# Performance work log

Measured on AMD Instinct MI355X. Metric: run time of the kernel, lower is better.

## Reference

```python
import jax, jax.numpy as jnp
import numpy as np


def setup_inputs() -> dict:
    key = jax.random.key(0)
    k1, k2 = jax.random.split(key)
    N, D, T = 1_000_000, 128, 1_000_000
    triplets = jax.random.randint(k1, (T, 3), 0, N, dtype=jnp.int64)
    node_emb = jax.random.normal(k2, (N, D), dtype=jnp.float32)
    vars = jnp.zeros((1,), dtype=jnp.float32)  # unused by forward (parity with original signature)
    return {"triplets": triplets, "node_emb": node_emb, "vars": vars}


def reference(triplets, node_emb, vars) -> jnp.ndarray:
    # gather left/right node embeddings, per-triplet dot product -> [T]
    left = node_emb[triplets[:, 0]]   # [T, D]
    right = node_emb[triplets[:, 2]]  # [T, D]
    scores = jnp.einsum('td,td->t', left, right)
    return scores
```

## Files before the change

### kernel.cpp

```cpp
#include <hip/hip_runtime.h>
#include <hip/hip_bf16.h>

constexpr int U = 8;

__global__ __launch_bounds__(256) void dot_gather_kernel(
    const int* __restrict__ trip,
    const float* __restrict__ emb,
    float* __restrict__ out,
    int T) {
  int gid = blockIdx.x * blockDim.x + threadIdx.x;
  int group = gid >> 5;
  int lane = gid & 31;
  long long t0 = (long long)group * U;
  if (t0 >= T) return;

  int iL[U], iR[U];
  #pragma unroll
  for (int u = 0; u < U; ++u) {
    long long t = (t0 + u < T) ? (t0 + u) : (long long)(T - 1);
    iL[u] = trip[3 * t];
    iR[u] = trip[3 * t + 2];
  }

  float4 a[U], b[U];
  #pragma unroll
  for (int u = 0; u < U; ++u) {
    a[u] = ((const float4*)(emb + (long long)iL[u] * 128))[lane];
    b[u] = ((const float4*)(emb + (long long)iR[u] * 128))[lane];
  }

  #pragma unroll
  for (int u = 0; u < U; ++u) {
    float s = a[u].x * b[u].x + a[u].y * b[u].y + a[u].z * b[u].z + a[u].w * b[u].w;
    #pragma unroll
    for (int off = 16; off > 0; off >>= 1)
      s += __shfl_down(s, off, 32);
    if (lane == 0 && t0 + u < T) out[t0 + u] = s;
  }
}

extern "C" void kernel_launch(void* const* d_in, const int* in_sizes, int n_in,
                              void* d_out, int out_size, void* d_ws, size_t ws_size,
                              hipStream_t stream) {
  const int* trip = (const int*)d_in[0];
  const float* emb = (const float*)d_in[1];
  float* out = (float*)d_out;

  int T = in_sizes[0] / 3;
  long long groups = ((long long)T + U - 1) / U;
  long long total_threads = groups * 32;
  int block = 256;
  long long grid = (total_threads + block - 1) / block;

  dot_gather_kernel<<<(int)grid, block, 0, stream>>>(trip, emb, out, T);
}
```

Baseline: 700.4 us.

## Convert embedding table to fp16 in workspace, then gather half-width rows

Adds a pre-pass that streams the full fp32 embedding table into an fp16 copy in workspace. The dot-product kernel then gathers 256-byte half rows, using 16 lanes per triplet instead of 32, and accumulates in fp32. The aim is to halve the random-gather traffic, which is the main cost. In exchange, every call pays a full-table read plus write in the conversion pass and loses input precision to fp16. There is an fp32 fallback path when workspace is too small.

```diff
diff --git a/kernel.cpp b/kernel.cpp
--- a/kernel.cpp
+++ b/kernel.cpp
@@ -1,17 +1,36 @@
 #include <hip/hip_runtime.h>
-#include <hip/hip_bf16.h>
+
+typedef _Float16 half8 __attribute__((ext_vector_type(8)));
+typedef float floatx4 __attribute__((ext_vector_type(4)));
 
 constexpr int U = 8;
 
-__global__ __launch_bounds__(256) void dot_gather_kernel(
+__global__ __launch_bounds__(256) void convert_f32_f16(
+    const float* __restrict__ emb, _Float16* __restrict__ h, long long n8) {
+  long long i = (long long)blockIdx.x * blockDim.x + threadIdx.x;
+  long long stride = (long long)gridDim.x * blockDim.x;
+  const floatx4* e4 = (const floatx4*)emb;
+  half8* h8 = (half8*)h;
+  for (long long k = i; k < n8; k += stride) {
+    floatx4 x = __builtin_nontemporal_load(&e4[2 * k]);
+    floatx4 y = __builtin_nontemporal_load(&e4[2 * k + 1]);
+    half8 v;
+    v[0] = (_Float16)x[0]; v[1] = (_Float16)x[1];
+    v[2] = (_Float16)x[2]; v[3] = (_Float16)x[3];
+    v[4] = (_Float16)y[0]; v[5] = (_Float16)y[1];
+    v[6] = (_Float16)y[2]; v[7] = (_Float16)y[3];
+    h8[k] = v;
+  }
+}
+
+__global__ __launch_bounds__(256) void dot_gather_f16(
     const int* __restrict__ trip,
-    const float* __restrict__ emb,
-    float* __restrict__ out,
-    int T) {
-  int gid = blockIdx.x * blockDim.x + threadIdx.x;
-  int group = gid >> 5;
-  int lane = gid & 31;
-  long long t0 = (long long)group * U;
+    const _Float16* __restrict__ h,
+    float* __restrict__ out, int T) {
+  long long gid = (long long)blockIdx.x * blockDim.x + threadIdx.x;
+  long long group = gid >> 4;
+  int lane = (int)(gid & 15);
+  long long t0 = group * U;
   if (t0 >= T) return;
 
   int iL[U], iR[U];
@@ -22,13 +41,48 @@
     iR[u] = trip[3 * t + 2];
   }
 
+  half8 a[U], b[U];
+  #pragma unroll
+  for (int u = 0; u < U; ++u) {
+    a[u] = ((const half8*)(h + (long long)iL[u] * 128))[lane];
+    b[u] = ((const half8*)(h + (long long)iR[u] * 128))[lane];
+  }
+
+  #pragma unroll
+  for (int u = 0; u < U; ++u) {
+    float s = 0.f;
+    #pragma unroll
+    for (int j = 0; j < 8; ++j)
+      s += (float)a[u][j] * (float)b[u][j];
+    #pragma unroll
+    for (int off = 8; off > 0; off >>= 1)
+      s += __shfl_down(s, off, 16);
+    if (lane == 0 && t0 + u < T)
+      __builtin_nontemporal_store(s, &out[t0 + u]);
+  }
+}
+
+__global__ __launch_bounds__(256) void dot_gather_f32(
+    const int* __restrict__ trip, const float* __restrict__ emb,
+    float* __restrict__ out, int T) {
+  int gid = blockIdx.x * blockDim.x + threadIdx.x;
+  int group = gid >> 5;
+  int lane = gid & 31;
+  long long t0 = (long long)group * U;
+  if (t0 >= T) return;
+  int iL[U], iR[U];
+  #pragma unroll
+  for (int u = 0; u < U; ++u) {
+    long long t = (t0 + u < T) ? (t0 + u) : (long long)(T - 1);
+    iL[u] = trip[3 * t];
+    iR[u] = trip[3 * t + 2];
+  }
   float4 a[U], b[U];
   #pragma unroll
   for (int u = 0; u < U; ++u) {
     a[u] = ((const float4*)(emb + (long long)iL[u] * 128))[lane];
     b[u] = ((const float4*)(emb + (long long)iR[u] * 128))[lane];
   }
-
   #pragma unroll
   for (int u = 0; u < U; ++u) {
     float s = a[u].x * b[u].x + a[u].y * b[u].y + a[u].z * b[u].z + a[u].w * b[u].w;
@@ -47,10 +101,24 @@
   float* out = (float*)d_out;
 
   int T = in_sizes[0] / 3;
-  long long groups = ((long long)T + U - 1) / U;
-  long long total_threads = groups * 32;
-  int block = 256;
-  long long grid = (total_threads + block - 1) / block;
+  long long nelem = (long long)in_sizes[1];
+  size_t need = (size_t)nelem * sizeof(_Float16);
 
-  dot_gather_kernel<<<(int)grid, block, 0, stream>>>(trip, emb, out, T);
+  if (ws_size >= need && (nelem & 7) == 0) {
+    _Float16* h = (_Float16*)d_ws;
+    long long n8 = nelem / 8;
+    convert_f32_f16<<<2048, 256, 0, stream>>>(emb, h, n8);
+
+    long long groups = ((long long)T + U - 1) / U;
+    long long total_threads = groups * 16;
+    int block = 256;
+    long long grid = (total_threads + block - 1) / block;
+    dot_gather_f16<<<(int)grid, block, 0, stream>>>(trip, h, out, T);
+  } else {
+    long long groups = ((long long)T + U - 1) / U;
+    long long total_threads = groups * 32;
+    int block = 256;
+    long long grid = (total_threads + block - 1) / block;
+    dot_gather_f32<<<(int)grid, block, 0, stream>>>(trip, emb, out, T);
+  }
 }
```

Result: slower. 739.3 us (+5.5%).
